# Optimization experiments

Measured on AMD Instinct MI355X. Metric: run time of the kernel, lower is better.

Reference implementation:

```python
import jax, jax.numpy as jnp
import numpy as np

B, S, D, H = 2, 2048, 1024, 16
DK = D // H


def setup_inputs() -> dict:
    key = jax.random.key(0)
    ks = jax.random.split(key, 8)
    xavier = lambda k, shape: jax.random.uniform(k, shape, jnp.float32, -1.0, 1.0) * np.sqrt(6.0 / (shape[0] + shape[1]))
    return {
        "query": jax.random.normal(ks[0], (B, S, D), jnp.float32),
        "key": jax.random.normal(ks[1], (B, S, D), jnp.float32),
        "value": jax.random.normal(ks[2], (B, S, D), jnp.float32),
        # causal mask: True above the diagonal -> masked out
        "mask": jnp.broadcast_to(jnp.triu(jnp.ones((S, S), bool), k=1), (B, S, S)),
        "w_q": xavier(ks[3], (D, D)),  # torch Linear weight [out, in]
        "w_k": xavier(ks[4], (D, D)),
        "w_v": xavier(ks[5], (D, D)),
        "w_o": xavier(ks[6], (D, D)),
        "b_o": jnp.zeros((D,), jnp.float32),
    }


def reference(query, key, value, mask, w_q, w_k, w_v, w_o, b_o):
    b, sq, d = query.shape
    sk = key.shape[1]
    # projections (torch Linear: x @ W.T)
    Q = (query @ w_q.T).reshape(b, sq, H, DK).transpose(0, 2, 1, 3)  # [B,H,Sq,DK]
    K = (key @ w_k.T).reshape(b, sk, H, DK).transpose(0, 2, 1, 3)
    V = (value @ w_v.T).reshape(b, sk, H, DK).transpose(0, 2, 1, 3)
    scores = jnp.einsum('bhqd,bhkd->bhqk', Q, K) / np.sqrt(DK)
    scores = jnp.where(mask[:, None, :, :], jnp.float32(-1e9), scores)
    attn = jax.nn.softmax(scores, axis=-1)  # dropout is identity in eval
    out = jnp.einsum('bhqk,bhkd->bhqd', attn, V)
    out = out.transpose(0, 2, 1, 3).reshape(b, sq, d)
    return out @ w_o.T + b_o
```

## Files before the change

kernel.cpp:

```cpp
#include <hip/hip_runtime.h>
#include <hip/hip_bf16.h>
#include <stdint.h>


typedef __attribute__((ext_vector_type(4))) float  f32x4;
typedef __attribute__((ext_vector_type(4))) int    i32x4;
typedef __attribute__((ext_vector_type(8))) __bf16 bf16x8;
typedef __attribute__((ext_vector_type(4))) __bf16 bf16x4;
typedef __attribute__((ext_vector_type(2))) __bf16 bf16x2;

#define MFMA16(a, b, c) __builtin_amdgcn_mfma_f32_16x16x32_bf16((a), (b), (c), 0, 0, 0)

__device__ __forceinline__ void async16(const void* g, void* lds) {
  __builtin_amdgcn_global_load_lds(
      (const __attribute__((address_space(1))) uint32_t*)g,
      (__attribute__((address_space(3))) uint32_t*)lds,
      16, 0, 0);
}

__device__ __forceinline__ bf16x8 lds_swz_read(const __bf16* base, int row, int cchunk) {
  const int sw = cchunk ^ (row & 7);
  return *(const bf16x8*)((const char*)base + row * 128 + sw * 16);
}

__global__ void detect_dtype(const uint16_t* __restrict__ w, int* __restrict__ flag) {
  __shared__ int s;
  if (threadIdx.x == 0) s = 0;
  __syncthreads();
  int big = 0;
  for (int i = threadIdx.x; i < 8192; i += 256) {
    uint32_t u = ((uint32_t)w[i]) << 16;
    float f;
    __builtin_memcpy(&f, &u, 4);
    if (fabsf(f) > 1.0f) big = 1;
  }
  if (big) atomicOr(&s, 1);
  __syncthreads();
  if (threadIdx.x == 0) *flag = s;
}

struct CvtArgs { const void* src[8]; void* dst[8]; int n[8]; };

__global__ __launch_bounds__(256)
void convert_all(CvtArgs a, const int* __restrict__ flagp) {
  if (*flagp == 0) return;
  const int t = blockIdx.y;
  const int n = a.n[t];
  const int i0 = (blockIdx.x * 256 + threadIdx.x) * 8;
  if (i0 >= n) return;
  const float* s = (const float*)a.src[t];
  __bf16* d = (__bf16*)a.dst[t];
  bf16x8 v;
#pragma unroll
  for (int j = 0; j < 8; ++j) v[j] = (__bf16)s[i0 + j];
  *(bf16x8*)(d + i0) = v;
}

struct GemmArgs {
  const __bf16* A[3];    const __bf16* W[3];
  const __bf16* Acvt[3]; const __bf16* Wcvt[3];
  void* C[3]; float scale[3];
  const __bf16* bias; const __bf16* biascvt;
  const int* flagp; int mode;
};

__global__ __launch_bounds__(256, 3)
void gemm_nt(GemmArgs ga)
{
  constexpr int K = 1024;
  __shared__ __align__(16) __bf16 smem[8704];
  __bf16* As = smem;
  __bf16* Bs = smem + 4096;

  const int id = blockIdx.x + (blockIdx.y << 3) + (blockIdx.z << 8);
  const int mb = (id & 7) * 4 + ((id >> 3) & 3);
  const int rest = id >> 5;
  const int nb = rest & 7;
  const int z = rest >> 3;

  const int f = *ga.flagp;
  const __bf16* __restrict__ A = f ? ga.Acvt[z] : ga.A[z];
  const __bf16* __restrict__ W = f ? ga.Wcvt[z] : ga.W[z];
  void* __restrict__ C = ga.C[z];
  const float scale = ga.scale[z];
  const int mode = ga.mode;

  const int tid = threadIdx.x;
  const int lane = tid & 63;
  const int wave = tid >> 6;
  const int l15 = lane & 15;
  const int quad = lane >> 4;
  const int bm = mb * 128;
  const int bn = nb * 128;
  const int wm = (wave >> 1) * 64;
  const int wn = (wave & 1) * 64;

  f32x4 acc[4][4];
#pragma unroll
  for (int mi = 0; mi < 4; ++mi)
#pragma unroll
    for (int ni = 0; ni < 4; ++ni) {
      f32x4 zz = {0.f, 0.f, 0.f, 0.f};
      acc[mi][ni] = zz;
    }

  for (int kt = 0; kt < K / 32; ++kt) {
    const int k0 = kt * 32;
    __syncthreads();
#pragma unroll
    for (int r = 0; r < 2; ++r) {
      const int chunk = r * 256 + wave * 64 + lane;
      const int row = chunk >> 2, c = chunk & 3;
      async16(A + (size_t)(bm + row) * K + k0 + c * 8, As + (r * 256 + wave * 64) * 8);
      async16(W + (size_t)(bn + row) * K + k0 + c * 8, Bs + (r * 256 + wave * 64) * 8);
    }
    __syncthreads();

    bf16x8 af[4];
    bf16x8 bfr[4];
#pragma unroll
    for (int mi = 0; mi < 4; ++mi)
      af[mi] = *(const bf16x8*)(As + (wm + mi * 16 + l15) * 32 + quad * 8);
#pragma unroll
    for (int ni = 0; ni < 4; ++ni)
      bfr[ni] = *(const bf16x8*)(Bs + (wn + ni * 16 + l15) * 32 + quad * 8);
#pragma unroll
    for (int mi = 0; mi < 4; ++mi)
#pragma unroll
      for (int ni = 0; ni < 4; ++ni)
        acc[mi][ni] = MFMA16(af[mi], bfr[ni], acc[mi][ni]);
  }

  float bv[4] = {0.f, 0.f, 0.f, 0.f};
  if (mode == 1) {
    const __bf16* bias = f ? ga.biascvt : ga.bias;
#pragma unroll
    for (int ni = 0; ni < 4; ++ni) bv[ni] = (float)bias[bn + wn + ni * 16 + l15];
  }
  __bf16 (*Cs)[136] = (__bf16(*)[136])smem;

#pragma unroll
  for (int pass = 0; pass < 2; ++pass) {
    __syncthreads();
    if ((wave >> 1) == pass) {
#pragma unroll
      for (int mi = 0; mi < 4; ++mi)
#pragma unroll
        for (int ni = 0; ni < 4; ++ni)
#pragma unroll
          for (int r = 0; r < 4; ++r)
            Cs[mi * 16 + quad * 4 + r][wn + ni * 16 + l15] =
                (__bf16)(acc[mi][ni][r] * scale + bv[ni]);
    }
    __syncthreads();

    if (mode == 0) {
#pragma unroll
      for (int it = 0; it < 4; ++it) {
        const int cid = it * 256 + tid;
        const int off = cid & 7, seg = cid >> 3;
        const int hl = seg & 1, rowl = seg >> 1;
        f32x4 v = *(const f32x4*)(&Cs[rowl][hl * 64 + off * 8]);
        const int m = bm + pass * 64 + rowl;
        const int b = m >> 11, s = m & 2047;
        const int h = (bn >> 6) + hl;
        *(f32x4*)((__bf16*)C + ((size_t)(b * 16 + h) * 2048 + s) * 64 + off * 8) = v;
      }
    } else if (f) {
#pragma unroll
      for (int it = 0; it < 4; ++it) {
        const int cid = it * 256 + tid;
        const int off = cid & 15, rowl = cid >> 4;
        bf16x8 vb = *(const bf16x8*)(&Cs[rowl][off * 8]);
        const int m = bm + pass * 64 + rowl;
        float* dst = (float*)C + (size_t)m * 1024 + bn + off * 8;
        f32x4 lo, hi;
#pragma unroll
        for (int j = 0; j < 4; ++j) { lo[j] = (float)vb[j]; hi[j] = (float)vb[4 + j]; }
        *(f32x4*)dst = lo;
        *(f32x4*)(dst + 4) = hi;
      }
    } else {
#pragma unroll
      for (int it = 0; it < 4; ++it) {
        const int cid = it * 256 + tid;
        const int off = cid & 15, rowl = cid >> 4;
        bf16x8 vb = *(const bf16x8*)(&Cs[rowl][off * 8]);
        const int m = bm + pass * 64 + rowl;
        *(bf16x8*)((__bf16*)C + (size_t)m * 1024 + bn + off * 8) = vb;
      }
    }
  }
}

__global__ __launch_bounds__(256, 3)
void attn(const __bf16* __restrict__ Q,
          const __bf16* __restrict__ Kg,
          const __bf16* __restrict__ Vg,
          __bf16* __restrict__ O)
{
  __shared__ __align__(16) __bf16 Ks[128 * 64];
  __shared__ __align__(16) __bf16 Vts[64][136];
  __shared__ __align__(16) __bf16 PsT[4][16][136];

  const int tid = threadIdx.x;
  const int lane = tid & 63;
  const int wave = tid >> 6;
  const int l15 = lane & 15;
  const int quad = lane >> 4;

  const int zb = blockIdx.x;
  const int qt = 31 - (zb >> 5);
  const int bh = zb & 31;
  const int q0 = qt * 64;
  const int nIter = (qt >> 1) + 1;

  const __bf16* Qp = Q + (size_t)bh * 2048 * 64;
  const __bf16* Kp = Kg + (size_t)bh * 2048 * 64;
  const __bf16* Vp = Vg + (size_t)bh * 2048 * 64;

  const int qrow_wl = wave * 16 + l15;

  bf16x8 qf[2];
#pragma unroll
  for (int kc = 0; kc < 2; ++kc)
    qf[kc] = *(const bf16x8*)(Qp + (size_t)(q0 + qrow_wl) * 64 + kc * 32 + quad * 8);

  f32x4 o_[4];
#pragma unroll
  for (int dt = 0; dt < 4; ++dt) {
    f32x4 zz = {0.f, 0.f, 0.f, 0.f};
    o_[dt] = zz;
  }
  float mrow = -1e30f, lrow = 0.0f;

  for (int ktt = 0; ktt < nIter; ++ktt) {
    const int k0 = ktt * 128;
    __syncthreads();
#pragma unroll
    for (int r = 0; r < 4; ++r) {
      const int chunk = r * 256 + tid;
      const int row = chunk >> 3, c = (chunk & 7) ^ (row & 7);
      async16(Kp + (size_t)(k0 + row) * 64 + c * 8,
              (char*)Ks + (r * 256 + wave * 64) * 16);
    }
#pragma unroll
    for (int rr = 0; rr < 2; ++rr) {
      const int task = rr * 256 + tid;
      const int pp = task & 63, dgg = task >> 6;
      bf16x8 v0 = *(const bf16x8*)(Vp + (size_t)(k0 + 2 * pp) * 64 + dgg * 8);
      bf16x8 v1 = *(const bf16x8*)(Vp + (size_t)(k0 + 2 * pp + 1) * 64 + dgg * 8);
#pragma unroll
      for (int j = 0; j < 8; ++j) {
        bf16x2 pr = { v0[j], v1[j] };
        *(bf16x2*)(&Vts[dgg * 8 + j][2 * pp]) = pr;
      }
    }
    __syncthreads();

    f32x4 st[8];
#pragma unroll
    for (int nt = 0; nt < 8; ++nt) {
      f32x4 zz = {0.f, 0.f, 0.f, 0.f};
      st[nt] = zz;
    }
#pragma unroll
    for (int kc = 0; kc < 2; ++kc)
#pragma unroll
      for (int nt = 0; nt < 8; ++nt) {
        bf16x8 kf = lds_swz_read(Ks, nt * 16 + l15, kc * 4 + quad);
        st[nt] = MFMA16(kf, qf[kc], st[nt]);
      }

    if (ktt == (qt >> 1)) {
#pragma unroll
      for (int nt = 0; nt < 8; ++nt)
#pragma unroll
        for (int r = 0; r < 4; ++r)
          if (k0 + nt * 16 + quad * 4 + r > q0 + qrow_wl) st[nt][r] = -1e30f;
    }

    float tmax = -1e30f;
#pragma unroll
    for (int nt = 0; nt < 8; ++nt)
#pragma unroll
      for (int r = 0; r < 4; ++r) tmax = fmaxf(tmax, st[nt][r]);
    tmax = fmaxf(tmax, __shfl_xor(tmax, 16, 64));
    tmax = fmaxf(tmax, __shfl_xor(tmax, 32, 64));
    const float mnew = fmaxf(mrow, tmax);
    const float alpha = __expf(mrow - mnew);
    float rs = 0.0f;
#pragma unroll
    for (int nt = 0; nt < 8; ++nt) {
      bf16x4 pd;
#pragma unroll
      for (int r = 0; r < 4; ++r) {
        const float pv = __expf(st[nt][r] - mnew);
        rs += pv;
        pd[r] = (__bf16)pv;
      }
      *(bf16x4*)(&PsT[wave][l15][nt * 16 + quad * 4]) = pd;
    }
    rs += __shfl_xor(rs, 16, 64);
    rs += __shfl_xor(rs, 32, 64);
    lrow = lrow * alpha + rs;
    mrow = mnew;
#pragma unroll
    for (int dt = 0; dt < 4; ++dt) o_[dt] *= alpha;

#pragma unroll
    for (int kc = 0; kc < 4; ++kc) {
      bf16x8 pf = *(const bf16x8*)(&PsT[wave][l15][kc * 32 + quad * 8]);
#pragma unroll
      for (int dt = 0; dt < 4; ++dt) {
        bf16x8 vf = *(const bf16x8*)(&Vts[dt * 16 + l15][kc * 32 + quad * 8]);
        o_[dt] = MFMA16(vf, pf, o_[dt]);
      }
    }
  }

  __syncthreads();
  __bf16 (*Ot)[72] = (__bf16(*)[72])&Vts[0][0];
  const float inv_l = 1.0f / lrow;
#pragma unroll
  for (int dt = 0; dt < 4; ++dt)
#pragma unroll
    for (int r = 0; r < 4; r += 2) {
      bf16x2 pr = { (__bf16)(o_[dt][r] * inv_l),
                    (__bf16)(o_[dt][r + 1] * inv_l) };
      *(bf16x2*)(&Ot[qrow_wl][dt * 16 + quad * 4 + r]) = pr;
    }
  __syncthreads();

  const int b = bh >> 4, h = bh & 15;
#pragma unroll
  for (int t = 0; t < 2; ++t) {
    const int i = t * 256 + tid;
    const int row = i >> 3, c = i & 7;
    f32x4 v = *(const f32x4*)(&Ot[row][c * 8]);
    *(f32x4*)(O + (size_t)(b * 2048 + q0 + row) * 1024 + h * 64 + c * 8) = v;
  }
}

extern "C" void kernel_launch(void* const* d_in, const int* in_sizes, int n_in,
                              void* d_out, int out_size, void* d_ws, size_t ws_size,
                              hipStream_t stream) {
  char* ws = (char*)d_ws;
  int* flag = (int*)ws;
  __bf16* Xc0 = (__bf16*)(ws + (1u << 20));
  __bf16* Xc1 = (__bf16*)(ws + (9u << 20));
  __bf16* Xc2 = (__bf16*)(ws + (17u << 20));
  __bf16* Wc0 = (__bf16*)(ws + (25u << 20));
  __bf16* Wc1 = (__bf16*)(ws + (27u << 20));
  __bf16* Wc2 = (__bf16*)(ws + (29u << 20));
  __bf16* Wc3 = (__bf16*)(ws + (31u << 20));
  __bf16* bc  = (__bf16*)(ws + (33u << 20));
  __bf16* Qw  = (__bf16*)(ws + (34u << 20));
  __bf16* Kw  = (__bf16*)(ws + (42u << 20));
  __bf16* Vw  = (__bf16*)(ws + (50u << 20));
  __bf16* Aw  = (__bf16*)(ws + (58u << 20));

  detect_dtype<<<1, 256, 0, stream>>>((const uint16_t*)d_in[4], flag);

  CvtArgs ca;
  ca.src[0] = d_in[0]; ca.dst[0] = Xc0; ca.n[0] = 4194304;
  ca.src[1] = d_in[1]; ca.dst[1] = Xc1; ca.n[1] = 4194304;
  ca.src[2] = d_in[2]; ca.dst[2] = Xc2; ca.n[2] = 4194304;
  ca.src[3] = d_in[4]; ca.dst[3] = Wc0; ca.n[3] = 1048576;
  ca.src[4] = d_in[5]; ca.dst[4] = Wc1; ca.n[4] = 1048576;
  ca.src[5] = d_in[6]; ca.dst[5] = Wc2; ca.n[5] = 1048576;
  ca.src[6] = d_in[7]; ca.dst[6] = Wc3; ca.n[6] = 1048576;
  ca.src[7] = d_in[8]; ca.dst[7] = bc;  ca.n[7] = 1024;
  convert_all<<<dim3(2048, 8), 256, 0, stream>>>(ca, flag);

  GemmArgs g0;
  g0.A[0] = (const __bf16*)d_in[0]; g0.Acvt[0] = Xc0;
  g0.A[1] = (const __bf16*)d_in[1]; g0.Acvt[1] = Xc1;
  g0.A[2] = (const __bf16*)d_in[2]; g0.Acvt[2] = Xc2;
  g0.W[0] = (const __bf16*)d_in[4]; g0.Wcvt[0] = Wc0;
  g0.W[1] = (const __bf16*)d_in[5]; g0.Wcvt[1] = Wc1;
  g0.W[2] = (const __bf16*)d_in[6]; g0.Wcvt[2] = Wc2;
  g0.C[0] = Qw; g0.scale[0] = 0.125f;
  g0.C[1] = Kw; g0.scale[1] = 1.0f;
  g0.C[2] = Vw; g0.scale[2] = 1.0f;
  g0.bias = nullptr; g0.biascvt = nullptr; g0.flagp = flag; g0.mode = 0;
  gemm_nt<<<dim3(8, 32, 3), 256, 0, stream>>>(g0);

  attn<<<dim3(1024), 256, 0, stream>>>(Qw, Kw, Vw, Aw);

  GemmArgs g1;
  g1.A[0] = Aw; g1.Acvt[0] = Aw;
  g1.A[1] = nullptr; g1.Acvt[1] = nullptr;
  g1.A[2] = nullptr; g1.Acvt[2] = nullptr;
  g1.W[0] = (const __bf16*)d_in[7]; g1.Wcvt[0] = Wc3;
  g1.W[1] = nullptr; g1.Wcvt[1] = nullptr;
  g1.W[2] = nullptr; g1.Wcvt[2] = nullptr;
  g1.C[0] = d_out; g1.scale[0] = 1.0f;
  g1.C[1] = nullptr; g1.scale[1] = 0.f;
  g1.C[2] = nullptr; g1.scale[2] = 0.f;
  g1.bias = (const __bf16*)d_in[8]; g1.biascvt = bc;
  g1.flagp = flag; g1.mode = 1;
  gemm_nt<<<dim3(8, 32, 1), 256, 0, stream>>>(g1);
}
```

Before: 241.6 us.

## Double-buffer K/V tiles with 64-key blocks and exp2 softmax in attention

The attention kernel now works on 64-key tiles instead of 128, which shrinks the LDS footprint and raises the occupancy target from 3 to 4 blocks per CU. K is double-buffered through async LDS loads, and the next V tile is prefetched into registers while the current tile is being computed. The softmax uses exp2 with log2(e) folded into the Q projection scale, and MFMA sections are wrapped in s_setprio. The cost is a second barrier per iteration and twice as many loop iterations. The causal diagonal now also falls on a 64-key boundary, so fewer masked keys are computed.

```diff
diff --git a/kernel.cpp b/kernel.cpp
--- a/kernel.cpp
+++ b/kernel.cpp
@@ -193,15 +193,15 @@
   }
 }
 
-__global__ __launch_bounds__(256, 3)
+__global__ __launch_bounds__(256, 4)
 void attn(const __bf16* __restrict__ Q,
           const __bf16* __restrict__ Kg,
           const __bf16* __restrict__ Vg,
           __bf16* __restrict__ O)
 {
-  __shared__ __align__(16) __bf16 Ks[128 * 64];
-  __shared__ __align__(16) __bf16 Vts[64][136];
-  __shared__ __align__(16) __bf16 PsT[4][16][136];
+  __shared__ __align__(16) __bf16 Ks[2][64 * 64];
+  __shared__ __align__(16) __bf16 Vts[64][72];
+  __shared__ __align__(16) __bf16 PsT[4][16][72];
 
   const int tid = threadIdx.x;
   const int lane = tid & 63;
@@ -213,7 +213,7 @@
   const int qt = 31 - (zb >> 5);
   const int bh = zb & 31;
   const int q0 = qt * 64;
-  const int nIter = (qt >> 1) + 1;
+  const int nIter = qt + 1;
 
   const __bf16* Qp = Q + (size_t)bh * 2048 * 64;
   const __bf16* Kp = Kg + (size_t)bh * 2048 * 64;
@@ -234,47 +234,63 @@
   }
   float mrow = -1e30f, lrow = 0.0f;
 
-  for (int ktt = 0; ktt < nIter; ++ktt) {
-    const int k0 = ktt * 128;
-    __syncthreads();
-#pragma unroll
-    for (int r = 0; r < 4; ++r) {
-      const int chunk = r * 256 + tid;
-      const int row = chunk >> 3, c = (chunk & 7) ^ (row & 7);
-      async16(Kp + (size_t)(k0 + row) * 64 + c * 8,
-              (char*)Ks + (r * 256 + wave * 64) * 16);
-    }
-#pragma unroll
-    for (int rr = 0; rr < 2; ++rr) {
-      const int task = rr * 256 + tid;
-      const int pp = task & 63, dgg = task >> 6;
-      bf16x8 v0 = *(const bf16x8*)(Vp + (size_t)(k0 + 2 * pp) * 64 + dgg * 8);
-      bf16x8 v1 = *(const bf16x8*)(Vp + (size_t)(k0 + 2 * pp + 1) * 64 + dgg * 8);
-#pragma unroll
-      for (int j = 0; j < 8; ++j) {
-        bf16x2 pr = { v0[j], v1[j] };
-        *(bf16x2*)(&Vts[dgg * 8 + j][2 * pp]) = pr;
-      }
-    }
-    __syncthreads();
-
-    f32x4 st[8];
-#pragma unroll
-    for (int nt = 0; nt < 8; ++nt) {
+  const int pp = tid & 31;
+  const int dgg = tid >> 5;
+
+#pragma unroll
+  for (int r = 0; r < 2; ++r) {
+    const int chunk = r * 256 + tid;
+    const int row = chunk >> 3, c = (chunk & 7) ^ (row & 7);
+    async16(Kp + (size_t)row * 64 + c * 8,
+            (char*)&Ks[0][0] + (r * 256 + wave * 64) * 16);
+  }
+  bf16x8 va = *(const bf16x8*)(Vp + (size_t)(2 * pp) * 64 + dgg * 8);
+  bf16x8 vb = *(const bf16x8*)(Vp + (size_t)(2 * pp + 1) * 64 + dgg * 8);
+
+  for (int t = 0; t < nIter; ++t) {
+    const int cur = t & 1;
+
+#pragma unroll
+    for (int j = 0; j < 8; ++j) {
+      bf16x2 pr = { va[j], vb[j] };
+      *(bf16x2*)(&Vts[dgg * 8 + j][2 * pp]) = pr;
+    }
+    __syncthreads();
+
+    bf16x8 vc = va, vd = vb;
+    if (t + 1 < nIter) {
+      const int k1 = (t + 1) * 64;
+#pragma unroll
+      for (int r = 0; r < 2; ++r) {
+        const int chunk = r * 256 + tid;
+        const int row = chunk >> 3, c = (chunk & 7) ^ (row & 7);
+        async16(Kp + (size_t)(k1 + row) * 64 + c * 8,
+                (char*)&Ks[cur ^ 1][0] + (r * 256 + wave * 64) * 16);
+      }
+      vc = *(const bf16x8*)(Vp + (size_t)(k1 + 2 * pp) * 64 + dgg * 8);
+      vd = *(const bf16x8*)(Vp + (size_t)(k1 + 2 * pp + 1) * 64 + dgg * 8);
+    }
+
+    f32x4 st[4];
+#pragma unroll
+    for (int nt = 0; nt < 4; ++nt) {
       f32x4 zz = {0.f, 0.f, 0.f, 0.f};
       st[nt] = zz;
     }
+    __builtin_amdgcn_s_setprio(1);
 #pragma unroll
     for (int kc = 0; kc < 2; ++kc)
 #pragma unroll
-      for (int nt = 0; nt < 8; ++nt) {
-        bf16x8 kf = lds_swz_read(Ks, nt * 16 + l15, kc * 4 + quad);
+      for (int nt = 0; nt < 4; ++nt) {
+        bf16x8 kf = lds_swz_read(&Ks[cur][0], nt * 16 + l15, kc * 4 + quad);
         st[nt] = MFMA16(kf, qf[kc], st[nt]);
       }
-
-    if (ktt == (qt >> 1)) {
-#pragma unroll
-      for (int nt = 0; nt < 8; ++nt)
+    __builtin_amdgcn_s_setprio(0);
+
+    if (t == qt) {
+      const int k0 = t * 64;
+#pragma unroll
+      for (int nt = 0; nt < 4; ++nt)
 #pragma unroll
         for (int r = 0; r < 4; ++r)
           if (k0 + nt * 16 + quad * 4 + r > q0 + qrow_wl) st[nt][r] = -1e30f;
@@ -282,20 +298,20 @@
 
     float tmax = -1e30f;
 #pragma unroll
-    for (int nt = 0; nt < 8; ++nt)
+    for (int nt = 0; nt < 4; ++nt)
 #pragma unroll
       for (int r = 0; r < 4; ++r) tmax = fmaxf(tmax, st[nt][r]);
     tmax = fmaxf(tmax, __shfl_xor(tmax, 16, 64));
     tmax = fmaxf(tmax, __shfl_xor(tmax, 32, 64));
     const float mnew = fmaxf(mrow, tmax);
-    const float alpha = __expf(mrow - mnew);
+    const float alpha = __builtin_amdgcn_exp2f(mrow - mnew);
     float rs = 0.0f;
 #pragma unroll
-    for (int nt = 0; nt < 8; ++nt) {
+    for (int nt = 0; nt < 4; ++nt) {
       bf16x4 pd;
 #pragma unroll
       for (int r = 0; r < 4; ++r) {
-        const float pv = __expf(st[nt][r] - mnew);
+        const float pv = __builtin_amdgcn_exp2f(st[nt][r] - mnew);
         rs += pv;
         pd[r] = (__bf16)pv;
       }
@@ -308,8 +324,9 @@
 #pragma unroll
     for (int dt = 0; dt < 4; ++dt) o_[dt] *= alpha;
 
-#pragma unroll
-    for (int kc = 0; kc < 4; ++kc) {
+    __builtin_amdgcn_s_setprio(1);
+#pragma unroll
+    for (int kc = 0; kc < 2; ++kc) {
       bf16x8 pf = *(const bf16x8*)(&PsT[wave][l15][kc * 32 + quad * 8]);
 #pragma unroll
       for (int dt = 0; dt < 4; ++dt) {
@@ -317,6 +334,10 @@
         o_[dt] = MFMA16(vf, pf, o_[dt]);
       }
     }
+    __builtin_amdgcn_s_setprio(0);
+
+    __syncthreads();
+    va = vc; vb = vd;
   }
 
   __syncthreads();
@@ -380,7 +401,7 @@
   g0.W[0] = (const __bf16*)d_in[4]; g0.Wcvt[0] = Wc0;
   g0.W[1] = (const __bf16*)d_in[5]; g0.Wcvt[1] = Wc1;
   g0.W[2] = (const __bf16*)d_in[6]; g0.Wcvt[2] = Wc2;
-  g0.C[0] = Qw; g0.scale[0] = 0.125f;
+  g0.C[0] = Qw; g0.scale[0] = 0.18033688f;
   g0.C[1] = Kw; g0.scale[1] = 1.0f;
   g0.C[2] = Vw; g0.scale[2] = 1.0f;
   g0.bias = nullptr; g0.biascvt = nullptr; g0.flagp = flag; g0.mode = 0;
```

After: 243.1 us. About the same (+0.7%).
